# Kernel optimization log

Measured on AMD Instinct MI355X. Metric: run time of the kernel, lower is better.

The kernel has to match this reference:

```python
import jax, jax.numpy as jnp
import numpy as np
from jax import lax

N = 8192
D = 128
CHUNK = 128  # rows of adj processed per scan step; bounds the [CHUNK, N, D] masked intermediate


def setup_inputs() -> dict:
    key = jax.random.key(0)
    k1, k2 = jax.random.split(key)
    x = jax.random.normal(k1, (N, D), dtype=jnp.float32)
    adj = jax.random.randint(k2, (N, N), 0, 2, dtype=jnp.int32)
    return {"x": x, "adj": adj}


def reference(x, adj):
    # For each node i: max over features of its neighbors (adj[i] nonzero),
    # or zeros if it has no neighbors. Equivalent to a masked row-max.
    n, d = x.shape
    neg = jnp.finfo(x.dtype).min
    adj_chunks = adj.reshape(n // CHUNK, CHUNK, n)

    def step(carry, a):  # a: [CHUNK, n]
        mask = a != 0
        # masked: [CHUNK, n, d] — neighbors keep x, non-neighbors get -inf-like
        masked = jnp.where(mask[:, :, None], x[None, :, :], neg)
        m = jnp.max(masked, axis=1)                      # [CHUNK, d]
        has_nbr = jnp.any(mask, axis=1)                  # [CHUNK]
        out = jnp.where(has_nbr[:, None], m, jnp.zeros((), x.dtype))
        return carry, out

    _, out = lax.scan(step, None, adj_chunks)
    return out.reshape(n, d)
```

## Files before the change

### kernel.cpp

```cpp
#include <hip/hip_runtime.h>
#include <cfloat>
#include <cstdint>

#define NN 8192
#define DD 128
#define WPR 256
#define TOPK 32

__device__ __forceinline__ uint32_t f2s(float f) {
  uint32_t u = __float_as_uint(f);
  return (u & 0x80000000u) ? ~u : (u | 0x80000000u);
}
__device__ __forceinline__ float s2f(uint32_t s) {
  return (s & 0x80000000u) ? __uint_as_float(s & 0x7fffffffu)
                           : __uint_as_float(~s);
}
__device__ __forceinline__ unsigned long long shfl_down_u64(unsigned long long v, int off) {
  unsigned lo = __shfl_down((unsigned)(v & 0xffffffffull), off, 64);
  unsigned hi = __shfl_down((unsigned)(v >> 32), off, 64);
  return ((unsigned long long)hi << 32) | (unsigned long long)lo;
}

__global__ __launch_bounds__(256) void prep_kernel(
    const float* __restrict__ x, const int* __restrict__ adj,
    uint32_t* __restrict__ bits, int* __restrict__ has_nbr,
    float* __restrict__ tkv, int* __restrict__ tki) {
  const int b = blockIdx.x;
  const int t = threadIdx.x;

  __shared__ unsigned long long red[4];
  __shared__ unsigned long long bcast;
  __shared__ int anyflag;

  if (b >= DD) {
    const int row = b - DD;
    const uint4* src = ((const uint4*)(adj + (size_t)row * NN)) + (size_t)t * 8;
    uint32_t w = 0;
#pragma unroll
    for (int c = 0; c < 8; ++c) {
      uint4 v = src[c];
      w |= (v.x ? 1u : 0u) << (4 * c + 0);
      w |= (v.y ? 1u : 0u) << (4 * c + 1);
      w |= (v.z ? 1u : 0u) << (4 * c + 2);
      w |= (v.w ? 1u : 0u) << (4 * c + 3);
    }
    bits[(size_t)row * WPR + t] = w;
    if (t == 0) anyflag = 0;
    __syncthreads();
    if (w) anyflag = 1;
    __syncthreads();
    if (t == 0) has_nbr[row] = anyflag;
  } else {
    const int d = b;
    float vals[32];
#pragma unroll
    for (int e = 0; e < 32; ++e) {
      int j = t * 32 + e;
      vals[e] = x[(size_t)j * DD + d];
    }
    unsigned long long prev = ~0ull;
    for (int k = 0; k < TOPK; ++k) {
      unsigned long long best = 0ull;
#pragma unroll
      for (int e = 0; e < 32; ++e) {
        int j = t * 32 + e;
        unsigned long long key =
            ((unsigned long long)f2s(vals[e]) << 32) | (unsigned)j;
        if (key < prev && key > best) best = key;
      }
      for (int off = 32; off; off >>= 1) {
        unsigned long long o = shfl_down_u64(best, off);
        if (o > best) best = o;
      }
      const int lane = t & 63, wv = t >> 6;
      if (lane == 0) red[wv] = best;
      __syncthreads();
      if (t == 0) {
        unsigned long long m = red[0];
        for (int i = 1; i < 4; ++i) if (red[i] > m) m = red[i];
        bcast = m;
        uint32_t s = (uint32_t)(m >> 32);
        uint32_t j = (uint32_t)(m & 0xffffffffu);
        tkv[k * DD + d] = s2f(s);
        tki[k * DD + d] = (int)j;
      }
      __syncthreads();
      prev = bcast;
    }
  }
}

__global__ __launch_bounds__(256) void probe_kernel(
    const float* __restrict__ x, const uint32_t* __restrict__ bits,
    const int* __restrict__ has_nbr, const float* __restrict__ tkv,
    const int* __restrict__ tki, float* __restrict__ out) {
  const int t = threadIdx.x;
  const int row = blockIdx.x * 2 + (t >> 7);
  const int d = t & 127;
  const uint32_t* rb = bits + (size_t)row * WPR;

  float res = 0.0f;
  bool done = false;
  for (int k = 0; k < TOPK; ++k) {
    int idx = tki[k * DD + d];
    float val = tkv[k * DD + d];
    uint32_t w = rb[idx >> 5];
    bool hit = (w >> (idx & 31)) & 1u;
    if (!done && hit) { res = val; done = true; }
    if (__all((int)done)) break;
  }
  if (__any((int)(!done))) {
    if (!done && has_nbr[row]) {
      float m = -FLT_MAX;
      for (int wd = 0; wd < WPR; ++wd) {
        uint32_t bm = rb[wd];
        while (bm) {
          int j = wd * 32 + __ffs(bm) - 1;
          bm &= bm - 1;
          m = fmaxf(m, x[(size_t)j * DD + d]);
        }
      }
      res = m;
    }
  }
  out[(size_t)row * DD + d] = res;
}

extern "C" void kernel_launch(void* const* d_in, const int* in_sizes, int n_in,
                              void* d_out, int out_size, void* d_ws, size_t ws_size,
                              hipStream_t stream) {
  const float* x = (const float*)d_in[0];
  const int* adj = (const int*)d_in[1];
  float* out = (float*)d_out;

  uint32_t* bits = (uint32_t*)d_ws;
  int* has_nbr = (int*)((char*)d_ws + (size_t)NN * WPR * 4);
  float* tkv = (float*)((char*)has_nbr + (size_t)NN * 4);
  int* tki = (int*)((char*)tkv + (size_t)TOPK * DD * 4);

  prep_kernel<<<NN + DD, 256, 0, stream>>>(x, adj, bits, has_nbr, tkv, tki);
  probe_kernel<<<NN / 2, 256, 0, stream>>>(x, bits, has_nbr, tkv, tki, out);
}
```

Before: 370.4 us.

## Pack adjacency bits via wavefront ballots with coalesced loads and prefetch probe words

The adjacency bit-packing now gives each wavefront one row. Lanes read consecutive uint4 chunks, so global loads are fully coalesced, and __ballot builds the bitmask in a permuted bit layout. This removes the per-block syncthreads, and has_nbr comes from the ballot OR. The probe kernel decodes the permuted layout and prefetches the first 12 top-k indices and bit words in an unrolled batch, hiding the latency of the serial dependent loads.

```diff
diff --git a/kernel.cpp b/kernel.cpp
--- a/kernel.cpp
+++ b/kernel.cpp
@@ -6,6 +6,7 @@
 #define DD 128
 #define WPR 256
 #define TOPK 32
+#define PRE 12
 
 __device__ __forceinline__ uint32_t f2s(float f) {
   uint32_t u = __float_as_uint(f);
@@ -21,6 +22,7 @@
   return ((unsigned long long)hi << 32) | (unsigned long long)lo;
 }
 
+
 __global__ __launch_bounds__(256) void prep_kernel(
     const float* __restrict__ x, const int* __restrict__ adj,
     uint32_t* __restrict__ bits, int* __restrict__ has_nbr,
@@ -30,26 +32,41 @@
 
   __shared__ unsigned long long red[4];
   __shared__ unsigned long long bcast;
-  __shared__ int anyflag;
 
   if (b >= DD) {
-    const int row = b - DD;
-    const uint4* src = ((const uint4*)(adj + (size_t)row * NN)) + (size_t)t * 8;
-    uint32_t w = 0;
+    const int lane = t & 63;
+    const int row = (b - DD) * 4 + (t >> 6);
+    const uint4* rp = (const uint4*)(adj + (size_t)row * NN);
+    uint32_t acc0 = 0, acc1 = 0, acc2 = 0, acc3 = 0;
+    unsigned long long any = 0ull;
+    const int oct = lane >> 3;
+    const int s = lane & 7;
 #pragma unroll
-    for (int c = 0; c < 8; ++c) {
-      uint4 v = src[c];
-      w |= (v.x ? 1u : 0u) << (4 * c + 0);
-      w |= (v.y ? 1u : 0u) << (4 * c + 1);
-      w |= (v.z ? 1u : 0u) << (4 * c + 2);
-      w |= (v.w ? 1u : 0u) << (4 * c + 3);
+    for (int g = 0; g < 32; ++g) {
+      uint4 v = rp[g * 64 + lane];
+      unsigned long long b0 = __ballot(v.x != 0);
+      unsigned long long b1 = __ballot(v.y != 0);
+      unsigned long long b2 = __ballot(v.z != 0);
+      unsigned long long b3 = __ballot(v.w != 0);
+      any |= (b0 | b1 | b2 | b3);
+      if (oct == (g & 7)) {
+        unsigned long long bb = (s & 4) ? ((s & 2) ? b3 : b2)
+                                        : ((s & 2) ? b1 : b0);
+        uint32_t word = (s & 1) ? (uint32_t)(bb >> 32) : (uint32_t)bb;
+        switch (g >> 3) {
+          case 0: acc0 = word; break;
+          case 1: acc1 = word; break;
+          case 2: acc2 = word; break;
+          case 3: acc3 = word; break;
+        }
+      }
     }
-    bits[(size_t)row * WPR + t] = w;
-    if (t == 0) anyflag = 0;
-    __syncthreads();
-    if (w) anyflag = 1;
-    __syncthreads();
-    if (t == 0) has_nbr[row] = anyflag;
+    uint32_t* ob = bits + (size_t)row * WPR;
+    ob[lane] = acc0;
+    ob[64 + lane] = acc1;
+    ob[128 + lane] = acc2;
+    ob[192 + lane] = acc3;
+    if (lane == 0) has_nbr[row] = (any != 0ull) ? 1 : 0;
   } else {
     const int d = b;
     float vals[32];
@@ -99,24 +116,41 @@
   const int d = t & 127;
   const uint32_t* rb = bits + (size_t)row * WPR;
 
+  int idxs[PRE];
+#pragma unroll
+  for (int k = 0; k < PRE; ++k) idxs[k] = tki[k * DD + d];
+  uint32_t wrd[PRE];
+#pragma unroll
+  for (int k = 0; k < PRE; ++k) {
+    int idx = idxs[k];
+    wrd[k] = rb[((idx >> 8) << 3) | ((idx & 3) << 1) | ((idx >> 7) & 1)];
+  }
   float res = 0.0f;
   bool done = false;
-  for (int k = 0; k < TOPK; ++k) {
+#pragma unroll
+  for (int k = 0; k < PRE; ++k) {
+    int idx = idxs[k];
+    bool hit = (wrd[k] >> ((idx >> 2) & 31)) & 1u;
+    if (!done && hit) { res = tkv[k * DD + d]; done = true; }
+  }
+  for (int k = PRE; k < TOPK; ++k) {
+    if (__all((int)done)) break;
     int idx = tki[k * DD + d];
     float val = tkv[k * DD + d];
-    uint32_t w = rb[idx >> 5];
-    bool hit = (w >> (idx & 31)) & 1u;
+    uint32_t w = rb[((idx >> 8) << 3) | ((idx & 3) << 1) | ((idx >> 7) & 1)];
+    bool hit = (w >> ((idx >> 2) & 31)) & 1u;
     if (!done && hit) { res = val; done = true; }
-    if (__all((int)done)) break;
   }
   if (__any((int)(!done))) {
     if (!done && has_nbr[row]) {
       float m = -FLT_MAX;
       for (int wd = 0; wd < WPR; ++wd) {
         uint32_t bm = rb[wd];
+        int base = ((wd >> 3) << 8) | ((wd & 1) << 7) | ((wd >> 1) & 3);
         while (bm) {
-          int j = wd * 32 + __ffs(bm) - 1;
+          int i = __ffs(bm) - 1;
           bm &= bm - 1;
+          int j = base + (i << 2);
           m = fmaxf(m, x[(size_t)j * DD + d]);
         }
       }
@@ -138,6 +172,6 @@
   float* tkv = (float*)((char*)has_nbr + (size_t)NN * 4);
   int* tki = (int*)((char*)tkv + (size_t)TOPK * DD * 4);
 
-  prep_kernel<<<NN + DD, 256, 0, stream>>>(x, adj, bits, has_nbr, tkv, tki);
+  prep_kernel<<<DD + NN / 4, 256, 0, stream>>>(x, adj, bits, has_nbr, tkv, tki);
   probe_kernel<<<NN / 2, 256, 0, stream>>>(x, bits, has_nbr, tkv, tki, out);
 }
```

Measured after the change: 375.2 us. No clear change (+1.3%).
